# Kernel optimization log

Measured on AMD Instinct MI355X. Metric: run time of the kernel, lower is better.

Reference implementation:

```python
import jax, jax.numpy as jnp
import numpy as np

N_NODES = 10000
N_REL = 500
H = 128
L = 128
EPS = 1e-12  # matches torch F.normalize eps


def _l2_normalize(x):
    # F.normalize(x, 2, -1): x / max(||x||_2, eps)
    n = jnp.sqrt(jnp.sum(x * x, axis=-1, keepdims=True))
    return x / jnp.maximum(n, EPS)


def setup_inputs() -> dict:
    key = jax.random.key(0)
    k1, k2, k3, k4 = jax.random.split(key, 4)
    return {
        "node_emb": jax.random.normal(k1, (N_NODES, H), dtype=jnp.float32),
        "rel_emb": jax.random.normal(k2, (N_REL, H), dtype=jnp.float32),
        "ent_idxs": jax.random.randint(k3, (L,), 0, N_NODES, dtype=jnp.int64 if jax.config.jax_enable_x64 else jnp.int32),
        "rel_idxs": jax.random.randint(k4, (L,), 0, N_REL, dtype=jnp.int64 if jax.config.jax_enable_x64 else jnp.int32),
    }


def reference(node_emb, rel_emb, ent_idxs, rel_idxs):
    # gather + L2 normalize  (TransE head+rel query vs all normalized entities)
    sel_ent = _l2_normalize(node_emb[ent_idxs])   # [L, H]
    sel_rel = _l2_normalize(rel_emb[rel_idxs])    # [L, H]
    all_ent = _l2_normalize(node_emb)             # [N, H]
    query = sel_ent + sel_rel                     # [L, H]
    # broadcasted difference instead of .repeat(): [L, N, H]
    diff = query[:, None, :] - all_ent[None, :, :]
    dist = jnp.sum(jnp.abs(diff), axis=-1)        # p_norm = 1 -> [L, N]
    # loss_name == 'BCELoss' -> softmax over all entities
    return jax.nn.softmax(dist, axis=-1)
```

## Files before the change

kernel.cpp:

```cpp
#include <hip/hip_runtime.h>
#include <math.h>

#define N_NODES 10000
#define N_REL   500
#define H       128
#define L       128

#define TN    20
#define NBLK  500

__device__ __forceinline__ float waveReduceSum(float v) {
    #pragma unroll
    for (int m = 1; m < 64; m <<= 1) v += __shfl_xor(v, m, 64);
    return v;
}

__device__ __forceinline__ void gload16(const float* g, float* l) {
    __builtin_amdgcn_global_load_lds((const __attribute__((address_space(1))) void*)g,
                                     (__attribute__((address_space(3))) void*)l, 16, 0, 0);
}

__global__ __launch_bounds__(256) void k_prep(const float* __restrict__ node,
                                              const float* __restrict__ rel,
                                              const int* __restrict__ eidx,
                                              const int* __restrict__ ridx,
                                              float* __restrict__ query) {
    int wav  = threadIdx.x >> 6;
    int lane = threadIdx.x & 63;
    int l = blockIdx.x * 4 + wav;
    int ei = eidx[l], ri = ridx[l];
    float2 e = *reinterpret_cast<const float2*>(node + ei * H + lane * 2);
    float inve = 1.0f / fmaxf(sqrtf(waveReduceSum(e.x * e.x + e.y * e.y)), 1e-12f);
    float2 r = *reinterpret_cast<const float2*>(rel + ri * H + lane * 2);
    float invr = 1.0f / fmaxf(sqrtf(waveReduceSum(r.x * r.x + r.y * r.y)), 1e-12f);
    float2 q;
    q.x = e.x * inve + r.x * invr;
    q.y = e.y * inve + r.y * invr;
    *reinterpret_cast<float2*>(query + l * H + lane * 2) = q;
}

__global__ __launch_bounds__(256, 2) void k_main(const float* __restrict__ node,
                                                 const float* __restrict__ query,
                                                 float* __restrict__ out,
                                                 float* __restrict__ psum) {
    __shared__ union {
        float qs[L * H];
        float red[4][128][21];
    } u;
    __shared__ float es[TN * H];
    __shared__ float invs[TN];

    const int tid  = threadIdx.x;
    const int w    = tid >> 6;
    const int lane = tid & 63;
    const int grp  = lane >> 2;
    const int nl   = lane & 3;
    const int nb   = blockIdx.x * TN;

    {
        const int c0   = (lane & 31) << 2;
        const int roff = lane >> 5;
        const int rq   = w * 32;
        #pragma unroll
        for (int k = 0; k < 16; ++k) {
            int r = rq + k * 2;
            int row = r + roff;
            int g = (row & 7) << 2;
            gload16(query + row * H + (c0 ^ g), &u.qs[r * H]);
        }
        #pragma unroll
        for (int k = 0; k < 10; ++k) {
            if ((k & 3) == w) {
                int r = k * 2;
                int row = r + roff;
                int g = (row & 7) << 2;
                gload16(node + (size_t)(nb + row) * H + (c0 ^ g), &es[r * H]);
            }
        }
    }
    __syncthreads();

    if (tid < 8 * TN) {
        int row = tid >> 3, seg = tid & 7;
        const float4* p = reinterpret_cast<const float4*>(es + row * H + seg * 16);
        float ss = 0.f;
        #pragma unroll
        for (int u2 = 0; u2 < 4; ++u2) {
            float4 v = p[u2];
            ss += v.x * v.x + v.y * v.y + v.z * v.z + v.w * v.w;
        }
        #pragma unroll
        for (int m = 1; m < 8; m <<= 1) ss += __shfl_xor(ss, m, 64);
        if (seg == 0) invs[row] = 1.0f / fmaxf(sqrtf(ss), 1e-12f);
    }
    __syncthreads();

    #pragma unroll
    for (int k = 0; k < 3; ++k) {
        int d4 = tid + (k << 8);
        if (d4 < TN * 32) {
            float s = invs[d4 >> 5];
            float4* p = reinterpret_cast<float4*>(es) + d4;
            float4 v = *p;
            v.x *= s; v.y *= s; v.z *= s; v.w *= s;
            *p = v;
        }
    }
    __syncthreads();

    const int gq = (grp & 7) << 2;
    int gej[5];
    #pragma unroll
    for (int j = 0; j < 5; ++j) gej[j] = ((nl + 4 * j) & 7) << 2;
    const int hs = w * 32;

    float acc[8][5] = {};

    #pragma unroll
    for (int hc = 0; hc < 8; ++hc) {
        const int h = hs + hc * 4;
        float4 qf[8], ef[5];
        #pragma unroll
        for (int i = 0; i < 8; ++i)
            qf[i] = *reinterpret_cast<const float4*>(&u.qs[(grp + 16 * i) * H + (h ^ gq)]);
        #pragma unroll
        for (int j = 0; j < 5; ++j)
            ef[j] = *reinterpret_cast<const float4*>(&es[(nl + 4 * j) * H + (h ^ gej[j])]);
        #pragma unroll
        for (int i = 0; i < 8; ++i)
            #pragma unroll
            for (int j = 0; j < 5; ++j)
                acc[i][j] += fabsf(qf[i].x - ef[j].x) + fabsf(qf[i].y - ef[j].y)
                           + fabsf(qf[i].z - ef[j].z) + fabsf(qf[i].w - ef[j].w);
    }

    __syncthreads();
    #pragma unroll
    for (int i = 0; i < 8; ++i)
        #pragma unroll
        for (int j = 0; j < 5; ++j)
            u.red[w][grp + 16 * i][nl + 4 * j] = acc[i][j];
    __syncthreads();

    {
        const int l  = tid >> 1;
        const int n0 = (tid & 1) * 10;
        float p[10];
        float rs = 0.f;
        #pragma unroll
        for (int k = 0; k < 10; ++k) {
            float d = u.red[0][l][n0 + k] + u.red[1][l][n0 + k]
                    + u.red[2][l][n0 + k] + u.red[3][l][n0 + k];
            p[k] = expf(d);
            rs += p[k];
        }
        float* po = out + (size_t)l * N_NODES + nb + n0;
        #pragma unroll
        for (int k = 0; k < 5; ++k)
            *reinterpret_cast<float2*>(po + 2 * k) = make_float2(p[2 * k], p[2 * k + 1]);
        rs += __shfl_xor(rs, 1, 64);
        if ((tid & 1) == 0) psum[l * NBLK + blockIdx.x] = rs;
    }
}

__global__ __launch_bounds__(256) void k_finish(float* __restrict__ out,
                                                const float* __restrict__ psum) {
    __shared__ float red[4];
    int l = blockIdx.y;
    int tid = threadIdx.x;
    const float* ps = psum + l * NBLK;
    float s = ps[tid] + (tid < NBLK - 256 ? ps[tid + 256] : 0.f);
    #pragma unroll
    for (int m = 1; m < 64; m <<= 1) s += __shfl_xor(s, m, 64);
    if ((tid & 63) == 0) red[tid >> 6] = s;
    __syncthreads();
    float inv = 1.0f / (red[0] + red[1] + red[2] + red[3]);

    int n4 = blockIdx.x * 256 + tid;
    if (n4 < 2500) {
        float4* o = reinterpret_cast<float4*>(out) + (size_t)l * 2500 + n4;
        float4 v = *o;
        v.x *= inv; v.y *= inv; v.z *= inv; v.w *= inv;
        *o = v;
    }
}

extern "C" void kernel_launch(void* const* d_in, const int* in_sizes, int n_in,
                              void* d_out, int out_size, void* d_ws, size_t ws_size,
                              hipStream_t stream) {
    const float* node = (const float*)d_in[0];
    const float* rel  = (const float*)d_in[1];
    const int*   eidx = (const int*)d_in[2];
    const int*   ridx = (const int*)d_in[3];
    float* out = (float*)d_out;

    float* query = (float*)d_ws;
    float* psum  = (float*)d_ws + 16384;

    k_prep<<<32, 256, 0, stream>>>(node, rel, eidx, ridx, query);
    k_main<<<NBLK, 256, 0, stream>>>(node, query, out, psum);

    dim3 gridC((2500 + 255) / 256, L);
    k_finish<<<gridC, 256, 0, stream>>>(out, psum);
}
```

Measured before the change: 27.18 us.

## Fuse query gather and normalization into main kernel, drop prep launch

```diff
diff --git a/kernel.cpp b/kernel.cpp
--- a/kernel.cpp
+++ b/kernel.cpp
@@ -8,6 +8,7 @@
 
 #define TN    20
 #define NBLK  500
+#define PSTR  512
 
 __device__ __forceinline__ float waveReduceSum(float v) {
     #pragma unroll
@@ -20,27 +21,10 @@
                                      (__attribute__((address_space(3))) void*)l, 16, 0, 0);
 }
 
-__global__ __launch_bounds__(256) void k_prep(const float* __restrict__ node,
-                                              const float* __restrict__ rel,
-                                              const int* __restrict__ eidx,
-                                              const int* __restrict__ ridx,
-                                              float* __restrict__ query) {
-    int wav  = threadIdx.x >> 6;
-    int lane = threadIdx.x & 63;
-    int l = blockIdx.x * 4 + wav;
-    int ei = eidx[l], ri = ridx[l];
-    float2 e = *reinterpret_cast<const float2*>(node + ei * H + lane * 2);
-    float inve = 1.0f / fmaxf(sqrtf(waveReduceSum(e.x * e.x + e.y * e.y)), 1e-12f);
-    float2 r = *reinterpret_cast<const float2*>(rel + ri * H + lane * 2);
-    float invr = 1.0f / fmaxf(sqrtf(waveReduceSum(r.x * r.x + r.y * r.y)), 1e-12f);
-    float2 q;
-    q.x = e.x * inve + r.x * invr;
-    q.y = e.y * inve + r.y * invr;
-    *reinterpret_cast<float2*>(query + l * H + lane * 2) = q;
-}
-
 __global__ __launch_bounds__(256, 2) void k_main(const float* __restrict__ node,
-                                                 const float* __restrict__ query,
+                                                 const float* __restrict__ rel,
+                                                 const int* __restrict__ eidx,
+                                                 const int* __restrict__ ridx,
                                                  float* __restrict__ out,
                                                  float* __restrict__ psum) {
     __shared__ union {
@@ -60,14 +44,6 @@
     {
         const int c0   = (lane & 31) << 2;
         const int roff = lane >> 5;
-        const int rq   = w * 32;
-        #pragma unroll
-        for (int k = 0; k < 16; ++k) {
-            int r = rq + k * 2;
-            int row = r + roff;
-            int g = (row & 7) << 2;
-            gload16(query + row * H + (c0 ^ g), &u.qs[r * H]);
-        }
         #pragma unroll
         for (int k = 0; k < 10; ++k) {
             if ((k & 3) == w) {
@@ -76,6 +52,42 @@
                 int g = (row & 7) << 2;
                 gload16(node + (size_t)(nb + row) * H + (c0 ^ g), &es[r * H]);
             }
+        }
+    }
+
+    #pragma unroll
+    for (int it = 0; it < 4; ++it) {
+        int row = it * 32 + (tid >> 3);
+        int seg = tid & 7;
+        int ei = eidx[row], ri = ridx[row];
+        const float4* pe = reinterpret_cast<const float4*>(node + (size_t)ei * H + seg * 16);
+        const float4* pr = reinterpret_cast<const float4*>(rel  + (size_t)ri * H + seg * 16);
+        float4 ev[4], rv[4];
+        #pragma unroll
+        for (int u2 = 0; u2 < 4; ++u2) { ev[u2] = pe[u2]; rv[u2] = pr[u2]; }
+        float se = 0.f, sr = 0.f;
+        #pragma unroll
+        for (int u2 = 0; u2 < 4; ++u2) {
+            se += ev[u2].x * ev[u2].x + ev[u2].y * ev[u2].y
+                + ev[u2].z * ev[u2].z + ev[u2].w * ev[u2].w;
+            sr += rv[u2].x * rv[u2].x + rv[u2].y * rv[u2].y
+                + rv[u2].z * rv[u2].z + rv[u2].w * rv[u2].w;
+        }
+        se += __shfl_xor(se, 1, 64); se += __shfl_xor(se, 2, 64); se += __shfl_xor(se, 4, 64);
+        sr += __shfl_xor(sr, 1, 64); sr += __shfl_xor(sr, 2, 64); sr += __shfl_xor(sr, 4, 64);
+        float inve = 1.0f / fmaxf(sqrtf(se), 1e-12f);
+        float invr = 1.0f / fmaxf(sqrtf(sr), 1e-12f);
+        int g = (row & 7) << 2;
+        float* dst = u.qs + row * H;
+        #pragma unroll
+        for (int u2 = 0; u2 < 4; ++u2) {
+            float4 q;
+            q.x = ev[u2].x * inve + rv[u2].x * invr;
+            q.y = ev[u2].y * inve + rv[u2].y * invr;
+            q.z = ev[u2].z * inve + rv[u2].z * invr;
+            q.w = ev[u2].w * inve + rv[u2].w * invr;
+            int c = (seg * 16 + u2 * 4) ^ g;
+            *reinterpret_cast<float4*>(dst + c) = q;
         }
     }
     __syncthreads();
@@ -159,7 +171,7 @@
         for (int k = 0; k < 5; ++k)
             *reinterpret_cast<float2*>(po + 2 * k) = make_float2(p[2 * k], p[2 * k + 1]);
         rs += __shfl_xor(rs, 1, 64);
-        if ((tid & 1) == 0) psum[l * NBLK + blockIdx.x] = rs;
+        if ((tid & 1) == 0) psum[l * PSTR + blockIdx.x] = rs;
     }
 }
 
@@ -168,7 +180,7 @@
     __shared__ float red[4];
     int l = blockIdx.y;
     int tid = threadIdx.x;
-    const float* ps = psum + l * NBLK;
+    const float* ps = psum + l * PSTR;
     float s = ps[tid] + (tid < NBLK - 256 ? ps[tid + 256] : 0.f);
     #pragma unroll
     for (int m = 1; m < 64; m <<= 1) s += __shfl_xor(s, m, 64);
@@ -194,11 +206,9 @@
     const int*   ridx = (const int*)d_in[3];
     float* out = (float*)d_out;
 
-    float* query = (float*)d_ws;
-    float* psum  = (float*)d_ws + 16384;
-
-    k_prep<<<32, 256, 0, stream>>>(node, rel, eidx, ridx, query);
-    k_main<<<NBLK, 256, 0, stream>>>(node, query, out, psum);
+    float* psum = (float*)d_ws;
+
+    k_main<<<NBLK, 256, 0, stream>>>(node, rel, eidx, ridx, out, psum);
 
     dim3 gridC((2500 + 255) / 256, L);
     k_finish<<<gridC, 256, 0, stream>>>(out, psum);
```

Result: no change. 27.03 us (-0.6%).

## Precompute entity inverse norms in prep kernel and read entity rows directly from global

Applied to the files above, without the earlier changes.

```diff
diff --git a/kernel.cpp b/kernel.cpp
--- a/kernel.cpp
+++ b/kernel.cpp
@@ -8,6 +8,7 @@
 
 #define TN    20
 #define NBLK  500
+#define PSTR  512
 
 __device__ __forceinline__ float waveReduceSum(float v) {
     #pragma unroll
@@ -24,22 +25,31 @@
                                               const float* __restrict__ rel,
                                               const int* __restrict__ eidx,
                                               const int* __restrict__ ridx,
+                                              float* __restrict__ invn,
                                               float* __restrict__ query) {
     int wav  = threadIdx.x >> 6;
     int lane = threadIdx.x & 63;
-    int l = blockIdx.x * 4 + wav;
-    int ei = eidx[l], ri = ridx[l];
-    float2 e = *reinterpret_cast<const float2*>(node + ei * H + lane * 2);
-    float inve = 1.0f / fmaxf(sqrtf(waveReduceSum(e.x * e.x + e.y * e.y)), 1e-12f);
-    float2 r = *reinterpret_cast<const float2*>(rel + ri * H + lane * 2);
-    float invr = 1.0f / fmaxf(sqrtf(waveReduceSum(r.x * r.x + r.y * r.y)), 1e-12f);
-    float2 q;
-    q.x = e.x * inve + r.x * invr;
-    q.y = e.y * inve + r.y * invr;
-    *reinterpret_cast<float2*>(query + l * H + lane * 2) = q;
+    if (blockIdx.x < 2500) {
+        int row = blockIdx.x * 4 + wav;
+        float2 v = *reinterpret_cast<const float2*>(node + row * H + lane * 2);
+        float ss = waveReduceSum(v.x * v.x + v.y * v.y);
+        if (lane == 0) invn[row] = 1.0f / fmaxf(sqrtf(ss), 1e-12f);
+    } else {
+        int l = (blockIdx.x - 2500) * 4 + wav;
+        int ei = eidx[l], ri = ridx[l];
+        float2 e = *reinterpret_cast<const float2*>(node + ei * H + lane * 2);
+        float inve = 1.0f / fmaxf(sqrtf(waveReduceSum(e.x * e.x + e.y * e.y)), 1e-12f);
+        float2 r = *reinterpret_cast<const float2*>(rel + ri * H + lane * 2);
+        float invr = 1.0f / fmaxf(sqrtf(waveReduceSum(r.x * r.x + r.y * r.y)), 1e-12f);
+        float2 q;
+        q.x = e.x * inve + r.x * invr;
+        q.y = e.y * inve + r.y * invr;
+        *reinterpret_cast<float2*>(query + l * H + lane * 2) = q;
+    }
 }
 
 __global__ __launch_bounds__(256, 2) void k_main(const float* __restrict__ node,
+                                                 const float* __restrict__ invn,
                                                  const float* __restrict__ query,
                                                  float* __restrict__ out,
                                                  float* __restrict__ psum) {
@@ -47,8 +57,6 @@
         float qs[L * H];
         float red[4][128][21];
     } u;
-    __shared__ float es[TN * H];
-    __shared__ float invs[TN];
 
     const int tid  = threadIdx.x;
     const int w    = tid >> 6;
@@ -56,6 +64,7 @@
     const int grp  = lane >> 2;
     const int nl   = lane & 3;
     const int nb   = blockIdx.x * TN;
+    const int hs   = w * 32;
 
     {
         const int c0   = (lane & 31) << 2;
@@ -68,64 +77,34 @@
             int g = (row & 7) << 2;
             gload16(query + row * H + (c0 ^ g), &u.qs[r * H]);
         }
-        #pragma unroll
-        for (int k = 0; k < 10; ++k) {
-            if ((k & 3) == w) {
-                int r = k * 2;
-                int row = r + roff;
-                int g = (row & 7) << 2;
-                gload16(node + (size_t)(nb + row) * H + (c0 ^ g), &es[r * H]);
-            }
-        }
     }
-    __syncthreads();
 
-    if (tid < 8 * TN) {
-        int row = tid >> 3, seg = tid & 7;
-        const float4* p = reinterpret_cast<const float4*>(es + row * H + seg * 16);
-        float ss = 0.f;
-        #pragma unroll
-        for (int u2 = 0; u2 < 4; ++u2) {
-            float4 v = p[u2];
-            ss += v.x * v.x + v.y * v.y + v.z * v.z + v.w * v.w;
-        }
-        #pragma unroll
-        for (int m = 1; m < 8; m <<= 1) ss += __shfl_xor(ss, m, 64);
-        if (seg == 0) invs[row] = 1.0f / fmaxf(sqrtf(ss), 1e-12f);
-    }
-    __syncthreads();
-
+    const float* eb[5];
+    float sj[5];
     #pragma unroll
-    for (int k = 0; k < 3; ++k) {
-        int d4 = tid + (k << 8);
-        if (d4 < TN * 32) {
-            float s = invs[d4 >> 5];
-            float4* p = reinterpret_cast<float4*>(es) + d4;
-            float4 v = *p;
-            v.x *= s; v.y *= s; v.z *= s; v.w *= s;
-            *p = v;
-        }
+    for (int j = 0; j < 5; ++j) {
+        int row = nb + nl + 4 * j;
+        eb[j] = node + (size_t)row * H + hs;
+        sj[j] = invn[row];
     }
     __syncthreads();
 
     const int gq = (grp & 7) << 2;
-    int gej[5];
-    #pragma unroll
-    for (int j = 0; j < 5; ++j) gej[j] = ((nl + 4 * j) & 7) << 2;
-    const int hs = w * 32;
-
     float acc[8][5] = {};
 
     #pragma unroll
     for (int hc = 0; hc < 8; ++hc) {
-        const int h = hs + hc * 4;
+        const int h = hs + (hc << 2);
         float4 qf[8], ef[5];
         #pragma unroll
         for (int i = 0; i < 8; ++i)
             qf[i] = *reinterpret_cast<const float4*>(&u.qs[(grp + 16 * i) * H + (h ^ gq)]);
         #pragma unroll
-        for (int j = 0; j < 5; ++j)
-            ef[j] = *reinterpret_cast<const float4*>(&es[(nl + 4 * j) * H + (h ^ gej[j])]);
+        for (int j = 0; j < 5; ++j) {
+            float4 t = *reinterpret_cast<const float4*>(eb[j] + (hc << 2));
+            ef[j].x = t.x * sj[j]; ef[j].y = t.y * sj[j];
+            ef[j].z = t.z * sj[j]; ef[j].w = t.w * sj[j];
+        }
         #pragma unroll
         for (int i = 0; i < 8; ++i)
             #pragma unroll
@@ -151,7 +130,7 @@
         for (int k = 0; k < 10; ++k) {
             float d = u.red[0][l][n0 + k] + u.red[1][l][n0 + k]
                     + u.red[2][l][n0 + k] + u.red[3][l][n0 + k];
-            p[k] = expf(d);
+            p[k] = __expf(d);
             rs += p[k];
         }
         float* po = out + (size_t)l * N_NODES + nb + n0;
@@ -159,7 +138,7 @@
         for (int k = 0; k < 5; ++k)
             *reinterpret_cast<float2*>(po + 2 * k) = make_float2(p[2 * k], p[2 * k + 1]);
         rs += __shfl_xor(rs, 1, 64);
-        if ((tid & 1) == 0) psum[l * NBLK + blockIdx.x] = rs;
+        if ((tid & 1) == 0) psum[l * PSTR + blockIdx.x] = rs;
     }
 }
 
@@ -168,7 +147,7 @@
     __shared__ float red[4];
     int l = blockIdx.y;
     int tid = threadIdx.x;
-    const float* ps = psum + l * NBLK;
+    const float* ps = psum + l * PSTR;
     float s = ps[tid] + (tid < NBLK - 256 ? ps[tid + 256] : 0.f);
     #pragma unroll
     for (int m = 1; m < 64; m <<= 1) s += __shfl_xor(s, m, 64);
@@ -194,11 +173,12 @@
     const int*   ridx = (const int*)d_in[3];
     float* out = (float*)d_out;
 
-    float* query = (float*)d_ws;
-    float* psum  = (float*)d_ws + 16384;
+    float* invn  = (float*)d_ws;
+    float* query = (float*)d_ws + 10240;
+    float* psum  = (float*)d_ws + 26624;
 
-    k_prep<<<32, 256, 0, stream>>>(node, rel, eidx, ridx, query);
-    k_main<<<NBLK, 256, 0, stream>>>(node, query, out, psum);
+    k_prep<<<2532, 256, 0, stream>>>(node, rel, eidx, ridx, invn, query);
+    k_main<<<NBLK, 256, 0, stream>>>(node, invn, query, out, psum);
 
     dim3 gridC((2500 + 255) / 256, L);
     k_finish<<<gridC, 256, 0, stream>>>(out, psum);
```

Measured after the change: 31.20 us. 1.15x slower.
